# Optimization experiments

Measured on AMD Instinct MI355X. Metric: run time of the kernel, lower is better.

The kernel has to match this reference:

```python
import jax, jax.numpy as jnp
import numpy as np

DIM = 512
CODEBOOK_SIZE = 8192
B, N = 4, 4096


def setup_inputs() -> dict:
    key = jax.random.key(0)
    k1, k2, k3 = jax.random.split(key, 3)
    scale = DIM ** -0.5
    x = jax.random.normal(k1, (B, N, DIM), dtype=jnp.float32)
    codebook = jax.random.normal(k2, (CODEBOOK_SIZE, DIM), dtype=jnp.float32) * scale
    W = jax.random.normal(k3, (DIM, DIM), dtype=jnp.float32) * scale  # Linear(dim, dim, bias=False) weight
    return {"x": x, "codebook": codebook, "W": W}


def reference(x, codebook, W):
    # implicit_codebook = Linear(codebook): codebook @ W.T   -> [C, D]
    implicit = codebook @ W.T

    # nearest-code search (no grad in original): squared euclidean distance
    x_sg = jax.lax.stop_gradient(x)
    imp_sg = jax.lax.stop_gradient(implicit)
    # [B, N, C] logits; ||x||^2 constant w.r.t. argmin so omitted
    d2 = jnp.sum(imp_sg * imp_sg, axis=-1) - 2.0 * jnp.einsum("bnd,cd->bnc", x_sg, imp_sg)
    indices = jnp.argmin(d2, axis=-1)  # [B, N]

    quantized = implicit[indices]  # gather [B, N, D]

    commit_loss = (
        0.25 * jnp.mean((x - jax.lax.stop_gradient(quantized)) ** 2)
        + jnp.mean((jax.lax.stop_gradient(x) - quantized) ** 2)
    )

    # straight-through estimator
    quantized_st = jax.lax.stop_gradient(quantized - x) + x
    return quantized_st, indices, commit_loss
```

## Files before the change

### kernel.cpp

```cpp
#include <hip/hip_runtime.h>
#include <stdint.h>

#define DIM 512
#define NCODE 8192
#define NTOK 16384
#define QELEMS (NTOK * DIM)
#define IDX_OFF QELEMS
#define LOSS_OFF (QELEMS + NTOK)

#define S_X 21.166666f
#define S_I 423.33334f
#define SXSI 8960.5551f
#define NQ_BIAS 131072
#define MARGIN_INT 3136

#define OFF_NORMS ((size_t)NCODE * DIM * 4)
#define OFF_XI8   (OFF_NORMS + (size_t)NCODE * 4)
#define OFF_II8   (OFF_XI8 + (size_t)NTOK * DIM)
#define OFF_CAND  (OFF_II8 + (size_t)NCODE * DIM)
#define OFF_NQ    (OFF_CAND + (size_t)NTOK * 64 * 4 * 4)

typedef short bf16x8 __attribute__((ext_vector_type(8)));
typedef float f32x4 __attribute__((ext_vector_type(4)));
typedef int   i32x4 __attribute__((ext_vector_type(4)));

__device__ inline unsigned ord32(float f) {
    unsigned u = __float_as_uint(f);
    return (u & 0x80000000u) ? ~u : (u | 0x80000000u);
}
__device__ inline unsigned short f2bf(float f) {
    unsigned u = __float_as_uint(f);
    return (unsigned short)((u + 0x7fffu + ((u >> 16) & 1u)) >> 16);
}
__device__ inline float bf2f(unsigned short h) {
    return __uint_as_float((unsigned)h << 16);
}
__device__ inline int q8(float v, float s) {
    return __float2int_rn(fminf(fmaxf(v * s, -127.f), 127.f));
}
__device__ inline void gl_lds16(const void* g, void* l) {
    __builtin_amdgcn_global_load_lds(
        (const __attribute__((address_space(1))) void*)g,
        (__attribute__((address_space(3))) void*)l, 16, 0, 0);
}

__global__ void init_kernel(float* __restrict__ norms) {
    int i = blockIdx.x * blockDim.x + threadIdx.x;
    if (i < NCODE) norms[i] = 0.f;
}

__global__ void split_kernel(const float* __restrict__ src,
                             unsigned short* __restrict__ dst, int n4) {
    int i = blockIdx.x * blockDim.x + threadIdx.x;
    if (i >= n4) return;
    float4 v = ((const float4*)src)[i];
    int r = i >> 7;
    int c = (i & 127) << 2;
    unsigned short hx = f2bf(v.x), hy = f2bf(v.y), hz = f2bf(v.z), hw = f2bf(v.w);
    ushort4 hi = {hx, hy, hz, hw};
    ushort4 lo = {f2bf(v.x - bf2f(hx)), f2bf(v.y - bf2f(hy)),
                  f2bf(v.z - bf2f(hz)), f2bf(v.w - bf2f(hw))};
    *(ushort4*)(dst + (size_t)r * 1024 + c) = hi;
    *(ushort4*)(dst + (size_t)r * 1024 + 512 + c) = lo;
}

__global__ __launch_bounds__(256, 2)
void gemm_imp_kernel(const unsigned short* __restrict__ A2,
                     const unsigned short* __restrict__ B2,
                     float* __restrict__ imp, unsigned char* __restrict__ impi8,
                     float* __restrict__ norms) {
    __shared__ __align__(16) unsigned short As2[64 * 64];
    __shared__ __align__(16) unsigned short Bs2[128 * 64];
    const int tid = threadIdx.x;
    const int l = tid & 63;
    const int w = tid >> 6;
    const int row0 = blockIdx.y * 64;
    const int col0 = blockIdx.x * 128;
    const int lr = l & 15;
    const int q = l >> 4;

    const int rr8 = l >> 3;
    const int gch = (l & 7) ^ (rr8 & 7);

    const unsigned short* gA = A2 + (size_t)(row0 + w * 8 + rr8) * 1024 + gch * 8;
    const unsigned short* gB = B2 + (size_t)(col0 + w * 8 + rr8) * 1024 + gch * 8;
    unsigned short* lA = As2 + (w * 8) * 64;
    unsigned short* lB = Bs2 + (w * 8) * 64;

    f32x4 acc[4][2];
    #pragma unroll
    for (int i = 0; i < 4; ++i)
        #pragma unroll
        for (int j = 0; j < 2; ++j) acc[i][j] = (f32x4)0.f;

    for (int c = 0; c < 32; ++c) {
        const int kA = (c & 15) << 6;
        const int kB = (c < 16) ? kA : ((kA + 512) & 1023);
        #pragma unroll
        for (int s = 0; s < 2; ++s)
            gl_lds16(gA + (size_t)(s * 32) * 1024 + kA, lA + (s * 32) * 64);
        #pragma unroll
        for (int s = 0; s < 4; ++s)
            gl_lds16(gB + (size_t)(s * 32) * 1024 + kB, lB + (s * 32) * 64);
        __syncthreads();
        #pragma unroll
        for (int ks = 0; ks < 2; ++ks) {
            const int lc = ks * 4 + q;
            bf16x8 af[4], bf[2];
            #pragma unroll
            for (int i = 0; i < 4; ++i) {
                const int ra = i * 16 + lr;
                af[i] = *(const bf16x8*)(As2 + ra * 64 + ((lc ^ (ra & 7)) << 3));
            }
            #pragma unroll
            for (int j = 0; j < 2; ++j) {
                const int rb = w * 32 + j * 16 + lr;
                bf[j] = *(const bf16x8*)(Bs2 + rb * 64 + ((lc ^ (rb & 7)) << 3));
            }
            #pragma unroll
            for (int i = 0; i < 4; ++i)
                #pragma unroll
                for (int j = 0; j < 2; ++j)
                    acc[i][j] = __builtin_amdgcn_mfma_f32_16x16x32_bf16(
                        af[i], bf[j], acc[i][j], 0, 0, 0);
        }
        __syncthreads();
    }

    #pragma unroll
    for (int i = 0; i < 4; ++i) {
        float np[4] = {0.f, 0.f, 0.f, 0.f};
        #pragma unroll
        for (int j = 0; j < 2; ++j) {
            const int col = col0 + w * 32 + j * 16 + lr;
            #pragma unroll
            for (int r = 0; r < 4; ++r) {
                const int row = row0 + i * 16 + q * 4 + r;
                const float v = acc[i][j][r];
                imp[(size_t)row * DIM + col] = v;
                impi8[(size_t)row * DIM + col] = (unsigned char)(q8(v, S_I) & 0xff);
                np[r] = fmaf(v, v, np[r]);
            }
        }
        #pragma unroll
        for (int r = 0; r < 4; ++r) {
            float s = np[r];
            #pragma unroll
            for (int m = 1; m < 16; m <<= 1) s += __shfl_xor(s, m, 64);
            if (lr == 0)
                atomicAdd(&norms[row0 + i * 16 + q * 4 + r], s);
        }
    }
}

__global__ void cvtx_kernel(const float* __restrict__ src,
                            unsigned char* __restrict__ dst,
                            const float* __restrict__ norms,
                            int* __restrict__ norms_q, int n4) {
    int i = blockIdx.x * blockDim.x + threadIdx.x;
    if (i >= n4) return;
    if (i < NCODE) norms_q[i] = __float2int_rn(norms[i] * SXSI) + NQ_BIAS;
    float4 v = ((const float4*)src)[i];
    unsigned wd = (unsigned)(q8(v.x, S_X) & 0xff)
                | ((unsigned)(q8(v.y, S_X) & 0xff) << 8)
                | ((unsigned)(q8(v.z, S_X) & 0xff) << 16)
                | ((unsigned)(q8(v.w, S_X) & 0xff) << 24);
    ((unsigned*)dst)[i] = wd;
}

__global__ __launch_bounds__(256, 4)
void coarse_kernel(const unsigned char* __restrict__ Xi8,
                   const unsigned char* __restrict__ Ii8,
                   const int* __restrict__ norms_q,
                   unsigned* __restrict__ cand) {
    __shared__ __align__(16) unsigned char smem[34816 + 4096];
    unsigned char* As = smem;
    unsigned char* Bsm = smem + 16384;
    unsigned (*S)[68] = (unsigned (*)[68])smem;
    unsigned* red = (unsigned*)(smem + 34816);

    const int tid = threadIdx.x;
    const int l = tid & 63;
    const int w = tid >> 6;

    const int id = blockIdx.y * 64 + blockIdx.x;
    const int xcd = id & 7;
    const int s8 = id >> 3;
    const int bx = xcd * 8 + (s8 & 7);
    const int by = s8 >> 3;
    const int row0 = by * 128;
    const int col0 = bx * 128;

    const int wm = w & 1, wn = w >> 1;
    const int lr = l & 15;
    const int q = l >> 4;

    const int rr8 = l >> 3;
    const int ch = (l & 7) ^ (rr8 & 7);
    const unsigned char* gA = Xi8 + (size_t)(row0 + w * 32 + rr8) * DIM + ch * 16;
    const unsigned char* gB = Ii8 + (size_t)(col0 + w * 32 + rr8) * DIM + ch * 16;
    unsigned char* lA = As + (w * 32) * 128;
    unsigned char* lB = Bsm + (w * 32) * 128;

    i32x4 acc[4][4];
    #pragma unroll
    for (int i = 0; i < 4; ++i)
        #pragma unroll
        for (int j = 0; j < 4; ++j) acc[i][j] = (i32x4)0;

    for (int kc = 0; kc < DIM; kc += 128) {
        #pragma unroll
        for (int s = 0; s < 4; ++s) {
            gl_lds16(gA + (size_t)(s * 8) * DIM + kc, lA + (s * 8) * 128);
            gl_lds16(gB + (size_t)(s * 8) * DIM + kc, lB + (s * 8) * 128);
        }
        __syncthreads();
        #pragma unroll
        for (int ks = 0; ks < 2; ++ks) {
            i32x4 af[4], bfr[4];
            #pragma unroll
            for (int i = 0; i < 4; ++i)
                af[i] = *(const i32x4*)(
                    As + (wm * 64 + i * 16 + lr) * 128 +
                    (((ks * 4 + q) ^ (lr & 7)) << 4));
            #pragma unroll
            for (int j = 0; j < 4; ++j)
                bfr[j] = *(const i32x4*)(
                    Bsm + (wn * 64 + j * 16 + lr) * 128 +
                    (((ks * 4 + q) ^ (lr & 7)) << 4));
            #pragma unroll
            for (int i = 0; i < 4; ++i)
                #pragma unroll
                for (int j = 0; j < 4; ++j)
                    acc[i][j] = __builtin_amdgcn_mfma_i32_16x16x64_i8(
                        af[i], bfr[j], acc[i][j], 0, 0, 0);
        }
        __syncthreads();
    }

    int nqo[4];
    unsigned codes[4];
    #pragma unroll
    for (int j = 0; j < 4; ++j) {
        codes[j] = (unsigned)(col0 + wn * 64 + j * 16 + lr);
        nqo[j] = norms_q[codes[j]];
    }
    #pragma unroll
    for (int i = 0; i < 4; ++i) {
        #pragma unroll
        for (int r = 0; r < 4; ++r) {
            unsigned pv[4];
            #pragma unroll
            for (int j = 0; j < 4; ++j) {
                int d2o = nqo[j] - 2 * acc[i][j][r];
                d2o = min(max(d2o, 0), 262143);
                pv[j] = ((unsigned)d2o << 13) | codes[j];
            }
            const unsigned s1 = min(pv[0], pv[1]), g1 = max(pv[0], pv[1]);
            const unsigned s2 = min(pv[2], pv[3]), g2 = max(pv[2], pv[3]);
            uint2 o;
            o.x = min(s1, s2);
            o.y = min(max(s1, s2), min(g1, g2));
            const int tok = wm * 64 + i * 16 + q * 4 + r;
            *(uint2*)&S[tok][wn * 32 + lr * 2] = o;
        }
    }
    __syncthreads();

    {
        const int t = tid & 127, h = tid >> 7;
        unsigned t0 = ~0u, t1 = ~0u, t2 = ~0u, t3 = ~0u;
        const uint4* sp = (const uint4*)&S[t][h * 32];
        #pragma unroll
        for (int ii = 0; ii < 8; ++ii) {
            const uint4 v4 = sp[ii];
            const unsigned vs[4] = {v4.x, v4.y, v4.z, v4.w};
            #pragma unroll
            for (int k = 0; k < 4; ++k) {
                const unsigned v = vs[k];
                if (v < t3) {
                    if (v < t2) {
                        t3 = t2;
                        if (v < t1) {
                            t2 = t1;
                            if (v < t0) { t1 = t0; t0 = v; } else t1 = v;
                        } else t2 = v;
                    } else t3 = v;
                }
            }
        }
        *(uint4*)&red[(t * 2 + h) * 4] = make_uint4(t0, t1, t2, t3);
    }
    __syncthreads();
    if (tid < 128) {
        const unsigned* a = &red[(tid * 2) * 4];
        const unsigned* b = &red[(tid * 2 + 1) * 4];
        uint4 o;
        o.x = min(a[0], b[3]); o.y = min(a[1], b[2]);
        o.z = min(a[2], b[1]); o.w = min(a[3], b[0]);
        *(uint4*)(cand + ((size_t)bx * NTOK + row0 + tid) * 4) = o;
    }
}

__global__ __launch_bounds__(256)
void merge_kernel(const float* __restrict__ X, const float* __restrict__ Imp,
                  const float* __restrict__ norms, const unsigned* __restrict__ cand,
                  float* __restrict__ out, float* __restrict__ lossp) {
    const int t = blockIdx.x * 4 + (threadIdx.x >> 6);
    const int l = threadIdx.x & 63;

    const uint4 c4 = *(const uint4*)(cand + ((size_t)l * NTOK + t) * 4);
    unsigned mn = min(min(c4.x, c4.y), min(c4.z, c4.w));
    #pragma unroll
    for (int o = 32; o > 0; o >>= 1)
        mn = min(mn, (unsigned)__shfl_xor((int)mn, o, 64));
    const unsigned th = (mn >> 13) + MARGIN_INT;

    const float4* xp = (const float4*)(X + (size_t)t * DIM);
    const float4 xa = xp[l * 2], xb = xp[l * 2 + 1];

    const unsigned vv[4] = {c4.x, c4.y, c4.z, c4.w};
    unsigned long long best = ~0ull;
    #pragma unroll
    for (int i = 0; i < 4; ++i) {
        const bool pass = (vv[i] >> 13) <= th;
        unsigned long long m = __ballot(pass);
        while (m) {
            const int src = __ffsll((unsigned long long)m) - 1;
            m &= m - 1;
            const int c = __shfl((int)(vv[i] & 8191u), src, 64);
            const float4* ip = (const float4*)(Imp + (size_t)c * DIM);
            const float4 ia = ip[l * 2], ib = ip[l * 2 + 1];
            float s = xa.x * ia.x + xa.y * ia.y + xa.z * ia.z + xa.w * ia.w
                    + xb.x * ib.x + xb.y * ib.y + xb.z * ib.z + xb.w * ib.w;
            #pragma unroll
            for (int o = 32; o > 0; o >>= 1) s += __shfl_xor(s, o, 64);
            const float d = fmaf(-2.f, s, norms[c]);
            const unsigned long long p =
                ((unsigned long long)ord32(d) << 32) | (unsigned)c;
            if (p < best) best = p;
        }
    }
    const int bi = (int)(best & 0xffffffffu);

    const float4* qp = (const float4*)(Imp + (size_t)bi * DIM);
    float4* op = (float4*)(out + (size_t)t * DIM);
    float ls = 0.f;
    #pragma unroll
    for (int jj = 0; jj < 2; ++jj) {
        const int j = l + jj * 64;
        const float4 qv = qp[j], xv = xp[j];
        op[j] = qv;
        const float dx = xv.x - qv.x, dy = xv.y - qv.y,
                    dz = xv.z - qv.z, dw = xv.w - qv.w;
        ls += dx * dx + dy * dy + dz * dz + dw * dw;
    }
    #pragma unroll
    for (int o = 32; o > 0; o >>= 1) ls += __shfl_xor(ls, o, 64);
    if (l == 0) {
        lossp[t] = ls;
        out[IDX_OFF + t] = (float)bi;
    }
}

__global__ __launch_bounds__(1024)
void fin_kernel(const float* __restrict__ lossp, float* __restrict__ out) {
    __shared__ float part[16];
    float s = 0.f;
    for (int i = threadIdx.x; i < NTOK; i += 1024) s += lossp[i];
    #pragma unroll
    for (int o = 32; o > 0; o >>= 1) s += __shfl_xor(s, o, 64);
    if ((threadIdx.x & 63) == 0) part[threadIdx.x >> 6] = s;
    __syncthreads();
    if (threadIdx.x == 0) {
        float tot = 0.f;
        #pragma unroll
        for (int i = 0; i < 16; ++i) tot += part[i];
        out[LOSS_OFF] = 1.25f * tot / (float)QELEMS;
    }
}

extern "C" void kernel_launch(void* const* d_in, const int* in_sizes, int n_in,
                              void* d_out, int out_size, void* d_ws, size_t ws_size,
                              hipStream_t stream) {
    const float* x  = (const float*)d_in[0];
    const float* cb = (const float*)d_in[1];
    const float* W  = (const float*)d_in[2];
    float* out = (float*)d_out;
    char* ws = (char*)d_ws;

    float* imp = (float*)ws;
    float* norms = (float*)(ws + OFF_NORMS);
    unsigned char* xi8 = (unsigned char*)(ws + OFF_XI8);
    unsigned char* ii8 = (unsigned char*)(ws + OFF_II8);
    unsigned* cand = (unsigned*)(ws + OFF_CAND);
    int* norms_q = (int*)(ws + OFF_NQ);
    unsigned short* cb2 = (unsigned short*)(ws + OFF_CAND);
    unsigned short* W2  = (unsigned short*)(ws + OFF_XI8);
    float* lossp = (float*)(ws + OFF_XI8);

    hipLaunchKernelGGL(init_kernel, dim3(NCODE / 256), dim3(256), 0, stream, norms);
    hipLaunchKernelGGL(split_kernel, dim3(NCODE * 128 / 256), dim3(256), 0, stream,
                       cb, cb2, NCODE * 128);
    hipLaunchKernelGGL(split_kernel, dim3(512 * 128 / 256), dim3(256), 0, stream,
                       W, W2, 512 * 128);
    hipLaunchKernelGGL(gemm_imp_kernel, dim3(DIM / 128, NCODE / 64), dim3(256), 0,
                       stream, cb2, W2, imp, ii8, norms);
    hipLaunchKernelGGL(cvtx_kernel, dim3(NTOK * DIM / 4 / 256), dim3(256), 0, stream,
                       x, xi8, norms, norms_q, NTOK * DIM / 4);
    hipLaunchKernelGGL(coarse_kernel, dim3(NCODE / 128, NTOK / 128), dim3(256), 0,
                       stream, xi8, ii8, norms_q, cand);
    hipLaunchKernelGGL(merge_kernel, dim3(NTOK / 4), dim3(256), 0, stream,
                       x, imp, norms, cand, out, lossp);
    hipLaunchKernelGGL(fin_kernel, dim3(1), dim3(1024), 0, stream, lossp, out);
}
```

Baseline: 252.8 us.

## Merge init/split launches, shrink implicit-codebook GEMM tile, coalesce merge loads

Folds the norm-zeroing and the two bf16 split launches into one kernel, cutting two launches. The codebook-times-W GEMM tile shrinks from 64x128 to 64x64 with a 2x2 wave layout and launch bounds raised to 4 blocks per SM. This doubles the grid for better occupancy, at the cost of loading each A tile twice as often. The merge kernel now reads x and implicit rows with a coalesced l / l+64 stride and reuses the loaded x values for the loss instead of reloading them.

```diff
diff --git a/kernel.cpp b/kernel.cpp
--- a/kernel.cpp
+++ b/kernel.cpp
@@ -20,6 +20,9 @@
 #define OFF_CAND  (OFF_II8 + (size_t)NCODE * DIM)
 #define OFF_NQ    (OFF_CAND + (size_t)NTOK * 64 * 4 * 4)
 
+#define N_CB4 (NCODE * 128)
+#define N_W4  (512 * 128)
+
 typedef short bf16x8 __attribute__((ext_vector_type(8)));
 typedef float f32x4 __attribute__((ext_vector_type(4)));
 typedef int   i32x4 __attribute__((ext_vector_type(4)));
@@ -44,18 +47,22 @@
         (__attribute__((address_space(3))) void*)l, 16, 0, 0);
 }
 
-__global__ void init_kernel(float* __restrict__ norms) {
+__global__ void split_kernel(const float* __restrict__ cb,
+                             const float* __restrict__ W,
+                             unsigned short* __restrict__ cb2,
+                             unsigned short* __restrict__ W2,
+                             float* __restrict__ norms) {
     int i = blockIdx.x * blockDim.x + threadIdx.x;
     if (i < NCODE) norms[i] = 0.f;
-}
-
-__global__ void split_kernel(const float* __restrict__ src,
-                             unsigned short* __restrict__ dst, int n4) {
-    int i = blockIdx.x * blockDim.x + threadIdx.x;
-    if (i >= n4) return;
-    float4 v = ((const float4*)src)[i];
-    int r = i >> 7;
-    int c = (i & 127) << 2;
+    const float4* src;
+    unsigned short* dst;
+    int idx;
+    if (i < N_CB4) { src = (const float4*)cb; dst = cb2; idx = i; }
+    else if (i < N_CB4 + N_W4) { src = (const float4*)W; dst = W2; idx = i - N_CB4; }
+    else return;
+    float4 v = src[idx];
+    int r = idx >> 7;
+    int c = (idx & 127) << 2;
     unsigned short hx = f2bf(v.x), hy = f2bf(v.y), hz = f2bf(v.z), hw = f2bf(v.w);
     ushort4 hi = {hx, hy, hz, hw};
     ushort4 lo = {f2bf(v.x - bf2f(hx)), f2bf(v.y - bf2f(hy)),
@@ -64,61 +71,60 @@
     *(ushort4*)(dst + (size_t)r * 1024 + 512 + c) = lo;
 }
 
-__global__ __launch_bounds__(256, 2)
+__global__ __launch_bounds__(256, 4)
 void gemm_imp_kernel(const unsigned short* __restrict__ A2,
                      const unsigned short* __restrict__ B2,
                      float* __restrict__ imp, unsigned char* __restrict__ impi8,
                      float* __restrict__ norms) {
     __shared__ __align__(16) unsigned short As2[64 * 64];
-    __shared__ __align__(16) unsigned short Bs2[128 * 64];
+    __shared__ __align__(16) unsigned short Bs2[64 * 64];
     const int tid = threadIdx.x;
     const int l = tid & 63;
     const int w = tid >> 6;
     const int row0 = blockIdx.y * 64;
-    const int col0 = blockIdx.x * 128;
+    const int col0 = blockIdx.x * 64;
+    const int wm = w & 1, wn = w >> 1;
     const int lr = l & 15;
     const int q = l >> 4;
 
     const int rr8 = l >> 3;
     const int gch = (l & 7) ^ (rr8 & 7);
 
-    const unsigned short* gA = A2 + (size_t)(row0 + w * 8 + rr8) * 1024 + gch * 8;
-    const unsigned short* gB = B2 + (size_t)(col0 + w * 8 + rr8) * 1024 + gch * 8;
-    unsigned short* lA = As2 + (w * 8) * 64;
-    unsigned short* lB = Bs2 + (w * 8) * 64;
-
-    f32x4 acc[4][2];
-    #pragma unroll
-    for (int i = 0; i < 4; ++i)
+    const unsigned short* gA = A2 + (size_t)(row0 + w * 16 + rr8) * 1024 + gch * 8;
+    const unsigned short* gB = B2 + (size_t)(col0 + w * 16 + rr8) * 1024 + gch * 8;
+    unsigned short* lA = As2 + (w * 16) * 64;
+    unsigned short* lB = Bs2 + (w * 16) * 64;
+
+    f32x4 acc[2][2];
+    #pragma unroll
+    for (int i = 0; i < 2; ++i)
         #pragma unroll
         for (int j = 0; j < 2; ++j) acc[i][j] = (f32x4)0.f;
 
     for (int c = 0; c < 32; ++c) {
         const int kA = (c & 15) << 6;
         const int kB = (c < 16) ? kA : ((kA + 512) & 1023);
-        #pragma unroll
-        for (int s = 0; s < 2; ++s)
-            gl_lds16(gA + (size_t)(s * 32) * 1024 + kA, lA + (s * 32) * 64);
-        #pragma unroll
-        for (int s = 0; s < 4; ++s)
-            gl_lds16(gB + (size_t)(s * 32) * 1024 + kB, lB + (s * 32) * 64);
+        gl_lds16(gA + kA, lA);
+        gl_lds16(gA + (size_t)8 * 1024 + kA, lA + 8 * 64);
+        gl_lds16(gB + kB, lB);
+        gl_lds16(gB + (size_t)8 * 1024 + kB, lB + 8 * 64);
         __syncthreads();
         #pragma unroll
         for (int ks = 0; ks < 2; ++ks) {
             const int lc = ks * 4 + q;
-            bf16x8 af[4], bf[2];
-            #pragma unroll
-            for (int i = 0; i < 4; ++i) {
-                const int ra = i * 16 + lr;
+            bf16x8 af[2], bf[2];
+            #pragma unroll
+            for (int i = 0; i < 2; ++i) {
+                const int ra = wm * 32 + i * 16 + lr;
                 af[i] = *(const bf16x8*)(As2 + ra * 64 + ((lc ^ (ra & 7)) << 3));
             }
             #pragma unroll
             for (int j = 0; j < 2; ++j) {
-                const int rb = w * 32 + j * 16 + lr;
+                const int rb = wn * 32 + j * 16 + lr;
                 bf[j] = *(const bf16x8*)(Bs2 + rb * 64 + ((lc ^ (rb & 7)) << 3));
             }
             #pragma unroll
-            for (int i = 0; i < 4; ++i)
+            for (int i = 0; i < 2; ++i)
                 #pragma unroll
                 for (int j = 0; j < 2; ++j)
                     acc[i][j] = __builtin_amdgcn_mfma_f32_16x16x32_bf16(
@@ -128,14 +134,14 @@
     }
 
     #pragma unroll
-    for (int i = 0; i < 4; ++i) {
+    for (int i = 0; i < 2; ++i) {
         float np[4] = {0.f, 0.f, 0.f, 0.f};
         #pragma unroll
         for (int j = 0; j < 2; ++j) {
-            const int col = col0 + w * 32 + j * 16 + lr;
+            const int col = col0 + wn * 32 + j * 16 + lr;
             #pragma unroll
             for (int r = 0; r < 4; ++r) {
-                const int row = row0 + i * 16 + q * 4 + r;
+                const int row = row0 + wm * 32 + i * 16 + q * 4 + r;
                 const float v = acc[i][j][r];
                 imp[(size_t)row * DIM + col] = v;
                 impi8[(size_t)row * DIM + col] = (unsigned char)(q8(v, S_I) & 0xff);
@@ -148,7 +154,7 @@
             #pragma unroll
             for (int m = 1; m < 16; m <<= 1) s += __shfl_xor(s, m, 64);
             if (lr == 0)
-                atomicAdd(&norms[row0 + i * 16 + q * 4 + r], s);
+                atomicAdd(&norms[row0 + wm * 32 + i * 16 + q * 4 + r], s);
         }
     }
 }
@@ -317,7 +323,7 @@
     const unsigned th = (mn >> 13) + MARGIN_INT;
 
     const float4* xp = (const float4*)(X + (size_t)t * DIM);
-    const float4 xa = xp[l * 2], xb = xp[l * 2 + 1];
+    const float4 xa = xp[l], xb = xp[l + 64];
 
     const unsigned vv[4] = {c4.x, c4.y, c4.z, c4.w};
     unsigned long long best = ~0ull;
@@ -330,7 +336,7 @@
             m &= m - 1;
             const int c = __shfl((int)(vv[i] & 8191u), src, 64);
             const float4* ip = (const float4*)(Imp + (size_t)c * DIM);
-            const float4 ia = ip[l * 2], ib = ip[l * 2 + 1];
+            const float4 ia = ip[l], ib = ip[l + 64];
             float s = xa.x * ia.x + xa.y * ia.y + xa.z * ia.z + xa.w * ia.w
                     + xb.x * ib.x + xb.y * ib.y + xb.z * ib.z + xb.w * ib.w;
             #pragma unroll
@@ -345,15 +351,16 @@
 
     const float4* qp = (const float4*)(Imp + (size_t)bi * DIM);
     float4* op = (float4*)(out + (size_t)t * DIM);
-    float ls = 0.f;
-    #pragma unroll
-    for (int jj = 0; jj < 2; ++jj) {
-        const int j = l + jj * 64;
-        const float4 qv = qp[j], xv = xp[j];
-        op[j] = qv;
-        const float dx = xv.x - qv.x, dy = xv.y - qv.y,
-                    dz = xv.z - qv.z, dw = xv.w - qv.w;
-        ls += dx * dx + dy * dy + dz * dz + dw * dw;
+    const float4 qa = qp[l], qb = qp[l + 64];
+    op[l] = qa; op[l + 64] = qb;
+    float ls;
+    {
+        const float dx0 = xa.x - qa.x, dy0 = xa.y - qa.y,
+                    dz0 = xa.z - qa.z, dw0 = xa.w - qa.w;
+        const float dx1 = xb.x - qb.x, dy1 = xb.y - qb.y,
+                    dz1 = xb.z - qb.z, dw1 = xb.w - qb.w;
+        ls = dx0 * dx0 + dy0 * dy0 + dz0 * dz0 + dw0 * dw0
+           + dx1 * dx1 + dy1 * dy1 + dz1 * dz1 + dw1 * dw1;
     }
     #pragma unroll
     for (int o = 32; o > 0; o >>= 1) ls += __shfl_xor(ls, o, 64);
@@ -399,12 +406,9 @@
     unsigned short* W2  = (unsigned short*)(ws + OFF_XI8);
     float* lossp = (float*)(ws + OFF_XI8);
 
-    hipLaunchKernelGGL(init_kernel, dim3(NCODE / 256), dim3(256), 0, stream, norms);
-    hipLaunchKernelGGL(split_kernel, dim3(NCODE * 128 / 256), dim3(256), 0, stream,
-                       cb, cb2, NCODE * 128);
-    hipLaunchKernelGGL(split_kernel, dim3(512 * 128 / 256), dim3(256), 0, stream,
-                       W, W2, 512 * 128);
-    hipLaunchKernelGGL(gemm_imp_kernel, dim3(DIM / 128, NCODE / 64), dim3(256), 0,
+    hipLaunchKernelGGL(split_kernel, dim3((N_CB4 + N_W4) / 256), dim3(256), 0, stream,
+                       cb, W, cb2, W2, norms);
+    hipLaunchKernelGGL(gemm_imp_kernel, dim3(DIM / 64, NCODE / 64), dim3(256), 0,
                        stream, cb2, W2, imp, ii8, norms);
     hipLaunchKernelGGL(cvtx_kernel, dim3(NTOK * DIM / 4 / 256), dim3(256), 0, stream,
                        x, xi8, norms, norms_q, NTOK * DIM / 4);
```

After: 254.7 us. Within noise of the previous version (+0.7%).
